# Optimization experiments

Measured on AMD Instinct MI355X. Metric: run time of the kernel, lower is better.

## Reference

```python
import jax, jax.numpy as jnp
import numpy as np

B, T, EMB, HS = 512, 256, 364, 64

def setup_inputs() -> dict:
    key = jax.random.key(0)
    ks = jax.random.split(key, 7)
    s = EMB ** -0.5  # keep weight scale sane
    return {
        "x": jax.random.normal(ks[0], (B, T, EMB), jnp.float32),
        "Wk": jax.random.normal(ks[1], (EMB, HS), jnp.float32) * s,
        "bk": jax.random.normal(ks[2], (HS,), jnp.float32) * 0.01,
        "Wq": jax.random.normal(ks[3], (EMB, HS), jnp.float32) * s,
        "bq": jax.random.normal(ks[4], (HS,), jnp.float32) * 0.01,
        "Wv": jax.random.normal(ks[5], (EMB, HS), jnp.float32) * s,
        "bv": jax.random.normal(ks[6], (HS,), jnp.float32) * 0.01,
    }

def reference(x, Wk, bk, Wq, bq, Wv, bv):
    # Faithful to the original: wei = k @ q^T (note swapped q/k vs textbook),
    # scaled by head_size**-0.5, causal mask, softmax, (dropout = identity in eval), then @ v.
    k = x @ Wk + bk          # [B, T, HS]
    q = x @ Wq + bq          # [B, T, HS]
    v = x @ Wv + bv          # [B, T, HS]
    scale = k.shape[-1] ** -0.5
    wei = jnp.einsum('btd,bsd->bts', k, q) * scale  # [B, T, T]
    causal = jnp.tril(jnp.ones((T, T), dtype=bool))
    wei = jnp.where(causal, wei, -jnp.inf)
    wei = jax.nn.softmax(wei, axis=-1)
    out = jnp.einsum('bts,bsd->btd', wei, v)        # [B, T, HS]
    return out
```

## Files before the change

### kernel.cpp

```cpp
#include <hip/hip_runtime.h>
#include <math.h>

#define BB   512
#define TT   256
#define EMBD 364
#define HS   64
#define KPAD 384
#define NC   192
#define XP   68

typedef __attribute__((ext_vector_type(8))) short short8_t;
typedef __attribute__((ext_vector_type(4))) float f32x4;

__device__ __forceinline__ ushort f2bf(float v) {
    union { float f; unsigned u; } c; c.f = v;
    unsigned b = c.u;
    return (ushort)((b + 0x7FFF + ((b >> 16) & 1)) >> 16);
}
__device__ __forceinline__ ushort f2bfc(float v) {
    union { float f; unsigned u; } c; c.f = v;
    return (ushort)((c.u + 0x8000u) >> 16);
}

#define GLOAD_LDS4(GP, LP)                                                        \
    __builtin_amdgcn_global_load_lds(                                             \
        (const __attribute__((address_space(1))) void*)(const void*)(GP),         \
        (__attribute__((address_space(3))) void*)(void*)(LP), 4, 0, 0)

#define WTR_BYTES ((size_t)144 * 512 * 2)
#define KQ_ELEMS  ((size_t)BB * TT * HS)
#define K_OFF_B   (WTR_BYTES)
#define Q_OFF_B   (K_OFF_B + KQ_ELEMS * 2)
#define VT_OFF_B  (Q_OFF_B + KQ_ELEMS * 2)

__global__ void prep_wtr(const float* __restrict__ Wk, const float* __restrict__ Wq,
                         const float* __restrict__ Wv, ushort* __restrict__ WTr)
{
    const int bid = blockIdx.x;
    const int jj  = bid / 12;
    const int t   = bid % 12;
    const int l   = threadIdx.x;
    const int c   = jj * 16 + (l & 15);
    const float* Wp = (c < 64) ? Wk : (c < 128 ? Wq : Wv);
    const float s   = (c < 64) ? 0.125f : 1.0f;
    const int col   = c & 63;
    #pragma unroll
    for (int i = 0; i < 8; ++i) {
        int k = t * 32 + (l >> 4) * 8 + i;
        float v = (k < EMBD) ? Wp[(size_t)k * HS + col] * s : 0.f;
        WTr[((size_t)bid * 64 + l) * 8 + i] = f2bf(v);
    }
}

__global__ __launch_bounds__(256, 2) void proj_gemm(
    const float* __restrict__ x, const ushort* __restrict__ WTr,
    const float* __restrict__ bk_, const float* __restrict__ bq_,
    const float* __restrict__ bv_,
    ushort* __restrict__ Kg, ushort* __restrict__ Qg, ushort* __restrict__ Vt)
{
    const int blk = blockIdx.x;
    const int tid = threadIdx.x;
    const int l   = tid & 63;
    const int w   = tid >> 6;
    const int l15 = l & 15;
    const int lg  = l >> 4;

    __shared__ float xf[2][64 * XP];

    const float* xb = x + (size_t)blk * 64 * EMBD;

    float bias3[3];
    #pragma unroll
    for (int j = 0; j < 3; ++j) {
        int c = w * 48 + j * 16 + l15;
        bias3[j] = (c < 64) ? bk_[c] * 0.125f : (c < 128 ? bq_[c - 64] : bv_[c - 128]);
    }

    f32x4 acc[4][3];
    #pragma unroll
    for (int mi = 0; mi < 4; ++mi)
        #pragma unroll
        for (int j = 0; j < 3; ++j) acc[mi][j] = (f32x4){0.f, 0.f, 0.f, 0.f};

    auto STAGE = [&](int kc, int buf) {
        const int colv = kc * 64 + l;
        const int col  = (colv < EMBD) ? colv : 0;
        #pragma unroll
        for (int rr = 0; rr < 16; ++rr) {
            const int row = w * 16 + rr;
            const float* gp = xb + (size_t)row * EMBD + col;
            GLOAD_LDS4(gp, &xf[buf][row * XP]);
        }
    };

    auto COMPUTE = [&](int kc, int buf) {
        short8_t Bf[3][2];
        #pragma unroll
        for (int j = 0; j < 3; ++j)
            #pragma unroll
            for (int ks = 0; ks < 2; ++ks)
                Bf[j][ks] = *(const short8_t*)&WTr[(((size_t)(w * 3 + j) * 12 + kc * 2 + ks) * 64 + l) * 8];
        short8_t a[4][2];
        #pragma unroll
        for (int mi = 0; mi < 4; ++mi)
            #pragma unroll
            for (int ks = 0; ks < 2; ++ks) {
                const float* p = &xf[buf][(mi * 16 + l15) * XP + ks * 32 + lg * 8];
                float4 p0 = *(const float4*)p;
                float4 p1 = *(const float4*)(p + 4);
                union { short8_t s8; ushort us[8]; } pk;
                pk.us[0] = f2bfc(p0.x); pk.us[1] = f2bfc(p0.y);
                pk.us[2] = f2bfc(p0.z); pk.us[3] = f2bfc(p0.w);
                pk.us[4] = f2bfc(p1.x); pk.us[5] = f2bfc(p1.y);
                pk.us[6] = f2bfc(p1.z); pk.us[7] = f2bfc(p1.w);
                a[mi][ks] = pk.s8;
            }
        #pragma unroll
        for (int ks = 0; ks < 2; ++ks)
            #pragma unroll
            for (int mi = 0; mi < 4; ++mi)
                #pragma unroll
                for (int j = 0; j < 3; ++j)
                    acc[mi][j] = __builtin_amdgcn_mfma_f32_16x16x32_bf16(a[mi][ks], Bf[j][ks], acc[mi][j], 0, 0, 0);
    };

    STAGE(0, 0);
    __syncthreads();
    #pragma unroll
    for (int kc = 0; kc < 6; ++kc) {
        if (kc < 5) STAGE(kc + 1, (kc + 1) & 1);
        COMPUTE(kc, kc & 1);
        __syncthreads();
    }

    const int b   = blk >> 2;
    const int tl0 = (blk & 3) * 64;
    #pragma unroll
    for (int j = 0; j < 3; ++j) {
        const int c = w * 48 + j * 16 + l15;
        #pragma unroll
        for (int mi = 0; mi < 4; ++mi) {
            if (c < 64) {
                #pragma unroll
                for (int r = 0; r < 4; ++r) {
                    const size_t trow = (size_t)blk * 64 + mi * 16 + lg * 4 + r;
                    Kg[trow * HS + c] = f2bf(acc[mi][j][r] + bias3[j]);
                }
            } else if (c < 128) {
                #pragma unroll
                for (int r = 0; r < 4; ++r) {
                    const size_t trow = (size_t)blk * 64 + mi * 16 + lg * 4 + r;
                    Qg[trow * HS + (c - 64)] = f2bf(acc[mi][j][r] + bias3[j]);
                }
            } else {
                ushort4 pk;
                pk.x = f2bf(acc[mi][j][0] + bias3[j]);
                pk.y = f2bf(acc[mi][j][1] + bias3[j]);
                pk.z = f2bf(acc[mi][j][2] + bias3[j]);
                pk.w = f2bf(acc[mi][j][3] + bias3[j]);
                *(ushort4*)&Vt[((size_t)b * HS + (c - 128)) * TT + tl0 + mi * 16 + lg * 4] = pk;
            }
        }
    }
}

__global__ __launch_bounds__(512, 4) void attn_fused(
    const ushort* __restrict__ Kg, const ushort* __restrict__ Qg,
    const ushort* __restrict__ Vt, float* __restrict__ out)
{
    const int b   = blockIdx.x;
    const int tid = threadIdx.x;
    const int l   = tid & 63;
    const int w   = tid >> 6;
    const int l15 = l & 15;
    const int lg  = l >> 4;

    __shared__ ushort pb[8][16 * 40];
    ushort* pbw = pb[w];

    const ushort* Kb = Kg + (size_t)b * TT * HS;
    const ushort* Qb = Qg + (size_t)b * TT * HS;
    const ushort* Vb = Vt + (size_t)b * HS * TT;

    #pragma unroll
    for (int half = 0; half < 2; ++half) {
        const int rt = half ? (15 - w) : w;
        const int t0 = rt * 16;

        short8_t afr[2];
        afr[0] = *(const short8_t*)&Kb[(t0 + l15) * HS + lg * 8];
        afr[1] = *(const short8_t*)&Kb[(t0 + l15) * HS + 32 + lg * 8];

        float mr[4], lr[4];
        f32x4 o[4];
        #pragma unroll
        for (int r = 0; r < 4; ++r) { mr[r] = -INFINITY; lr[r] = 0.f; }
        #pragma unroll
        for (int nt = 0; nt < 4; ++nt) o[nt] = (f32x4){0.f, 0.f, 0.f, 0.f};

        const int jd = t0 >> 5;
        for (int j = 0; j <= jd; ++j) {
            const int sb = j * 32;
            f32x4 sacc[2];
            sacc[0] = (f32x4){0.f, 0.f, 0.f, 0.f};
            sacc[1] = (f32x4){0.f, 0.f, 0.f, 0.f};
            #pragma unroll
            for (int kk = 0; kk < 2; ++kk) {
                #pragma unroll
                for (int ct = 0; ct < 2; ++ct) {
                    short8_t bfr = *(const short8_t*)&Qb[(sb + ct * 16 + l15) * HS + kk * 32 + lg * 8];
                    sacc[ct] = __builtin_amdgcn_mfma_f32_16x16x32_bf16(afr[kk], bfr, sacc[ct], 0, 0, 0);
                }
            }
            #pragma unroll
            for (int ct = 0; ct < 2; ++ct) {
                int s = sb + ct * 16 + l15;
                #pragma unroll
                for (int r = 0; r < 4; ++r) {
                    int t = t0 + lg * 4 + r;
                    if (s > t) sacc[ct][r] = -INFINITY;
                }
            }
            float p0[4], p1[4], fsc[4];
            #pragma unroll
            for (int r = 0; r < 4; ++r) {
                float mx = fmaxf(sacc[0][r], sacc[1][r]);
                mx = fmaxf(mx, __shfl_xor(mx, 1));
                mx = fmaxf(mx, __shfl_xor(mx, 2));
                mx = fmaxf(mx, __shfl_xor(mx, 4));
                mx = fmaxf(mx, __shfl_xor(mx, 8));
                float nm = fmaxf(mr[r], mx);
                fsc[r] = __expf(mr[r] - nm);
                mr[r] = nm;
                p0[r] = __expf(sacc[0][r] - nm);
                p1[r] = __expf(sacc[1][r] - nm);
                float ps = p0[r] + p1[r];
                ps += __shfl_xor(ps, 1);
                ps += __shfl_xor(ps, 2);
                ps += __shfl_xor(ps, 4);
                ps += __shfl_xor(ps, 8);
                lr[r] = lr[r] * fsc[r] + ps;
            }
            #pragma unroll
            for (int nt = 0; nt < 4; ++nt)
                #pragma unroll
                for (int r = 0; r < 4; ++r) o[nt][r] *= fsc[r];
            #pragma unroll
            for (int r = 0; r < 4; ++r) {
                pbw[(lg * 4 + r) * 40 + l15]      = f2bf(p0[r]);
                pbw[(lg * 4 + r) * 40 + 16 + l15] = f2bf(p1[r]);
            }
            short8_t pa = *(const short8_t*)&pbw[l15 * 40 + lg * 8];
            #pragma unroll
            for (int nt = 0; nt < 4; ++nt) {
                short8_t bfr = *(const short8_t*)&Vb[(nt * 16 + l15) * TT + sb + lg * 8];
                o[nt] = __builtin_amdgcn_mfma_f32_16x16x32_bf16(pa, bfr, o[nt], 0, 0, 0);
            }
        }
        #pragma unroll
        for (int r = 0; r < 4; ++r) {
            float inv = 1.0f / lr[r];
            int t = t0 + lg * 4 + r;
            float* op = out + ((size_t)b * TT + t) * HS;
            #pragma unroll
            for (int nt = 0; nt < 4; ++nt)
                op[nt * 16 + l15] = o[nt][r] * inv;
        }
    }
}

extern "C" void kernel_launch(void* const* d_in, const int* in_sizes, int n_in,
                              void* d_out, int out_size, void* d_ws, size_t ws_size,
                              hipStream_t stream) {
    const float* x  = (const float*)d_in[0];
    const float* Wk = (const float*)d_in[1];
    const float* bk = (const float*)d_in[2];
    const float* Wq = (const float*)d_in[3];
    const float* bq = (const float*)d_in[4];
    const float* Wv = (const float*)d_in[5];
    const float* bv = (const float*)d_in[6];
    float* out = (float*)d_out;

    ushort* WTr = (ushort*)d_ws;
    ushort* Kg  = (ushort*)((char*)d_ws + K_OFF_B);
    ushort* Qg  = (ushort*)((char*)d_ws + Q_OFF_B);
    ushort* Vt  = (ushort*)((char*)d_ws + VT_OFF_B);

    prep_wtr<<<dim3(144), dim3(64), 0, stream>>>(Wk, Wq, Wv, WTr);
    proj_gemm<<<dim3(2048), dim3(256), 0, stream>>>(x, WTr, bk, bq, bv, Kg, Qg, Vt);
    attn_fused<<<dim3(BB), dim3(512), 0, stream>>>(Kg, Qg, Vt, out);
}
```

Before: 109.6 us.

## Load whole 32-row x tile at once with 16-byte LDS DMA and XOR swizzle

The projection GEMM now handles 32 rows per block instead of 64, doubling the grid to 4096 blocks. Each block loads its entire 32x384 x tile into LDS up front using 16-byte global_load_lds transfers with an XOR-swizzled column layout, replacing the double-buffered 4-byte-per-lane staging loop. Occupancy hint rises to 3 blocks per SIMD pair. This targets the load instruction count and the per-chunk barriers, at the cost of no overlap between load and compute inside a block, and half the reuse of each weight fragment load.

```diff
diff --git a/kernel.cpp b/kernel.cpp
--- a/kernel.cpp
+++ b/kernel.cpp
@@ -7,7 +7,6 @@
 #define HS   64
 #define KPAD 384
 #define NC   192
-#define XP   68
 
 typedef __attribute__((ext_vector_type(8))) short short8_t;
 typedef __attribute__((ext_vector_type(4))) float f32x4;
@@ -22,10 +21,10 @@
     return (ushort)((c.u + 0x8000u) >> 16);
 }
 
-#define GLOAD_LDS4(GP, LP)                                                        \
+#define GLOAD_LDS16(GP, LP)                                                       \
     __builtin_amdgcn_global_load_lds(                                             \
         (const __attribute__((address_space(1))) void*)(const void*)(GP),         \
-        (__attribute__((address_space(3))) void*)(void*)(LP), 4, 0, 0)
+        (__attribute__((address_space(3))) void*)(void*)(LP), 16, 0, 0)
 
 #define WTR_BYTES ((size_t)144 * 512 * 2)
 #define KQ_ELEMS  ((size_t)BB * TT * HS)
@@ -52,7 +51,7 @@
     }
 }
 
-__global__ __launch_bounds__(256, 2) void proj_gemm(
+__global__ __launch_bounds__(256, 3) void proj_gemm(
     const float* __restrict__ x, const ushort* __restrict__ WTr,
     const float* __restrict__ bk_, const float* __restrict__ bq_,
     const float* __restrict__ bv_,
@@ -65,9 +64,21 @@
     const int l15 = l & 15;
     const int lg  = l >> 4;
 
-    __shared__ float xf[2][64 * XP];
-
-    const float* xb = x + (size_t)blk * 64 * EMBD;
+    __shared__ float xf[32 * KPAD];
+
+    const float* xb = x + (size_t)blk * 32 * EMBD;
+
+    #pragma unroll
+    for (int gi = 0; gi < 12; ++gi) {
+        const int g     = w * 12 + gi;
+        const unsigned flatP = (unsigned)(g * 64 + l);
+        const unsigned row   = flatP / 96u;
+        const unsigned p     = flatP % 96u;
+        const unsigned q     = p ^ (row & 7u);
+        const unsigned colq  = (q < 91u) ? q : 0u;
+        const float* gp = xb + (size_t)row * EMBD + colq * 4u;
+        GLOAD_LDS16(gp, (char*)xf + (size_t)g * 1024);
+    }
 
     float bias3[3];
     #pragma unroll
@@ -76,80 +87,56 @@
         bias3[j] = (c < 64) ? bk_[c] * 0.125f : (c < 128 ? bq_[c - 64] : bv_[c - 128]);
     }
 
-    f32x4 acc[4][3];
-    #pragma unroll
-    for (int mi = 0; mi < 4; ++mi)
+    f32x4 acc[2][3];
+    #pragma unroll
+    for (int mi = 0; mi < 2; ++mi)
         #pragma unroll
         for (int j = 0; j < 3; ++j) acc[mi][j] = (f32x4){0.f, 0.f, 0.f, 0.f};
 
-    auto STAGE = [&](int kc, int buf) {
-        const int colv = kc * 64 + l;
-        const int col  = (colv < EMBD) ? colv : 0;
-        #pragma unroll
-        for (int rr = 0; rr < 16; ++rr) {
-            const int row = w * 16 + rr;
-            const float* gp = xb + (size_t)row * EMBD + col;
-            GLOAD_LDS4(gp, &xf[buf][row * XP]);
-        }
-    };
-
-    auto COMPUTE = [&](int kc, int buf) {
-        short8_t Bf[3][2];
+    __syncthreads();
+
+    #pragma unroll
+    for (int ks = 0; ks < 12; ++ks) {
+        short8_t Bf[3];
         #pragma unroll
         for (int j = 0; j < 3; ++j)
-            #pragma unroll
-            for (int ks = 0; ks < 2; ++ks)
-                Bf[j][ks] = *(const short8_t*)&WTr[(((size_t)(w * 3 + j) * 12 + kc * 2 + ks) * 64 + l) * 8];
-        short8_t a[4][2];
-        #pragma unroll
-        for (int mi = 0; mi < 4; ++mi)
-            #pragma unroll
-            for (int ks = 0; ks < 2; ++ks) {
-                const float* p = &xf[buf][(mi * 16 + l15) * XP + ks * 32 + lg * 8];
-                float4 p0 = *(const float4*)p;
-                float4 p1 = *(const float4*)(p + 4);
-                union { short8_t s8; ushort us[8]; } pk;
-                pk.us[0] = f2bfc(p0.x); pk.us[1] = f2bfc(p0.y);
-                pk.us[2] = f2bfc(p0.z); pk.us[3] = f2bfc(p0.w);
-                pk.us[4] = f2bfc(p1.x); pk.us[5] = f2bfc(p1.y);
-                pk.us[6] = f2bfc(p1.z); pk.us[7] = f2bfc(p1.w);
-                a[mi][ks] = pk.s8;
-            }
-        #pragma unroll
-        for (int ks = 0; ks < 2; ++ks)
-            #pragma unroll
-            for (int mi = 0; mi < 4; ++mi)
-                #pragma unroll
-                for (int j = 0; j < 3; ++j)
-                    acc[mi][j] = __builtin_amdgcn_mfma_f32_16x16x32_bf16(a[mi][ks], Bf[j][ks], acc[mi][j], 0, 0, 0);
-    };
-
-    STAGE(0, 0);
-    __syncthreads();
-    #pragma unroll
-    for (int kc = 0; kc < 6; ++kc) {
-        if (kc < 5) STAGE(kc + 1, (kc + 1) & 1);
-        COMPUTE(kc, kc & 1);
-        __syncthreads();
-    }
-
-    const int b   = blk >> 2;
-    const int tl0 = (blk & 3) * 64;
+            Bf[j] = *(const short8_t*)&WTr[(((size_t)(w * 3 + j) * 12 + ks) * 64 + l) * 8];
+        #pragma unroll
+        for (int mi = 0; mi < 2; ++mi) {
+            const unsigned row = mi * 16 + l15;
+            const unsigned q0  = ks * 8 + lg * 2;
+            const unsigned p0  = q0 ^ (row & 7u);
+            const unsigned p1  = (q0 + 1u) ^ (row & 7u);
+            f32x4 A0 = *(const f32x4*)&xf[row * KPAD + p0 * 4u];
+            f32x4 A1 = *(const f32x4*)&xf[row * KPAD + p1 * 4u];
+            union { short8_t s8; ushort us[8]; } pk;
+            pk.us[0] = f2bfc(A0[0]); pk.us[1] = f2bfc(A0[1]);
+            pk.us[2] = f2bfc(A0[2]); pk.us[3] = f2bfc(A0[3]);
+            pk.us[4] = f2bfc(A1[0]); pk.us[5] = f2bfc(A1[1]);
+            pk.us[6] = f2bfc(A1[2]); pk.us[7] = f2bfc(A1[3]);
+            #pragma unroll
+            for (int j = 0; j < 3; ++j)
+                acc[mi][j] = __builtin_amdgcn_mfma_f32_16x16x32_bf16(pk.s8, Bf[j], acc[mi][j], 0, 0, 0);
+        }
+    }
+
+    const int b   = blk >> 3;
+    const int tl0 = (blk & 7) * 32;
     #pragma unroll
     for (int j = 0; j < 3; ++j) {
         const int c = w * 48 + j * 16 + l15;
         #pragma unroll
-        for (int mi = 0; mi < 4; ++mi) {
+        for (int mi = 0; mi < 2; ++mi) {
             if (c < 64) {
                 #pragma unroll
                 for (int r = 0; r < 4; ++r) {
-                    const size_t trow = (size_t)blk * 64 + mi * 16 + lg * 4 + r;
+                    const size_t trow = (size_t)blk * 32 + mi * 16 + lg * 4 + r;
                     Kg[trow * HS + c] = f2bf(acc[mi][j][r] + bias3[j]);
                 }
             } else if (c < 128) {
                 #pragma unroll
                 for (int r = 0; r < 4; ++r) {
-                    const size_t trow = (size_t)blk * 64 + mi * 16 + lg * 4 + r;
+                    const size_t trow = (size_t)blk * 32 + mi * 16 + lg * 4 + r;
                     Qg[trow * HS + (c - 64)] = f2bf(acc[mi][j][r] + bias3[j]);
                 }
             } else {
@@ -287,6 +274,6 @@
     ushort* Vt  = (ushort*)((char*)d_ws + VT_OFF_B);
 
     prep_wtr<<<dim3(144), dim3(64), 0, stream>>>(Wk, Wq, Wv, WTr);
-    proj_gemm<<<dim3(2048), dim3(256), 0, stream>>>(x, WTr, bk, bq, bv, Kg, Qg, Vt);
+    proj_gemm<<<dim3(4096), dim3(256), 0, stream>>>(x, WTr, bk, bq, bv, Kg, Qg, Vt);
     attn_fused<<<dim3(BB), dim3(512), 0, stream>>>(Kg, Qg, Vt, out);
 }
```

Result: slower. 112.2 us (median of 3 runs) (+2.4%).
